# Kernel optimization log

Hardware: AMD Instinct MI355X
Metric: run time of the kernel (lower is better)

The kernel has to match this reference:

```python
import jax, jax.numpy as jnp
import numpy as np

B, NQ, NK, C = 8, 1024, 1024, 1024
H, DK, DV = 16, 64, 64


def setup_inputs() -> dict:
    key = jax.random.key(0)
    ks = jax.random.split(key, 10)
    queries = jax.random.normal(ks[0], (B, NQ, C), dtype=jnp.float32)
    keys_ = jax.random.normal(ks[1], (B, NK, C), dtype=jnp.float32)
    values = jax.random.normal(ks[2], (B, NK, C), dtype=jnp.float32)
    attention_mask = jax.random.randint(ks[3], (B, H, NQ, NK), 0, 2).astype(jnp.bool_)
    attention_weights = jax.random.uniform(ks[4], (B, H, NQ, NK), dtype=jnp.float32)
    std = 0.001  # init.normal_(m.weight, std=0.001), bias=0
    Wq = jax.random.normal(ks[5], (C, H * DK), dtype=jnp.float32) * std
    Wk = jax.random.normal(ks[6], (C, H * DK), dtype=jnp.float32) * std
    Wv = jax.random.normal(ks[7], (C, H * DV), dtype=jnp.float32) * std
    Wo = jax.random.normal(ks[8], (H * DV, C), dtype=jnp.float32) * std
    bq = jnp.zeros((H * DK,), jnp.float32)
    bk = jnp.zeros((H * DK,), jnp.float32)
    bv = jnp.zeros((H * DV,), jnp.float32)
    bo = jnp.zeros((C,), jnp.float32)
    return {"queries": queries, "keys": keys_, "values": values,
            "attention_mask": attention_mask, "attention_weights": attention_weights,
            "Wq": Wq, "bq": bq, "Wk": Wk, "bk": bk, "Wv": Wv, "bv": bv,
            "Wo": Wo, "bo": bo}


def reference(queries, keys, values, attention_mask, attention_weights,
              Wq, bq, Wk, bk, Wv, bv, Wo, bo):
    bs, nq, _ = queries.shape
    nk = keys.shape[1]
    # projections -> (b, h, n, d)
    q = (queries @ Wq + bq).reshape(bs, nq, H, DK).transpose(0, 2, 1, 3)
    k = (keys @ Wk + bk).reshape(bs, nk, H, DK).transpose(0, 2, 1, 3)
    v = (values @ Wv + bv).reshape(bs, nk, H, DV).transpose(0, 2, 1, 3)
    att = jnp.einsum('bhqd,bhkd->bhqk', q, k) / np.sqrt(DK).astype(np.float32)
    att = att * attention_weights
    att = jnp.where(attention_mask, -jnp.inf, att)
    att = jax.nn.softmax(att, axis=-1)
    # dropout is identity in eval mode
    out = jnp.einsum('bhqk,bhkd->bhqd', att, v)
    out = out.transpose(0, 2, 1, 3).reshape(bs, nq, H * DV)
    return out @ Wo + bo
```

## Files before the change

kernel.cpp:

```cpp
#include <hip/hip_runtime.h>
#include <hip/hip_bf16.h>

using short8 = __attribute__((ext_vector_type(8))) short;
using f32x4  = __attribute__((ext_vector_type(4))) float;

__device__ __forceinline__ unsigned short f2bf(float f) {
    union { float f; unsigned u; } x; x.f = f;
    unsigned r = x.u + 0x7FFFu + ((x.u >> 16) & 1u);
    return (unsigned short)(r >> 16);
}

__device__ __forceinline__ void gload_lds16(const void* g, void* l) {
    __builtin_amdgcn_global_load_lds(
        (const __attribute__((address_space(1))) unsigned int*)g,
        (__attribute__((address_space(3))) unsigned int*)l, 16, 0, 0);
}

__global__ void detect_mask_kernel(const unsigned int* __restrict__ m, int* __restrict__ flag) {
    if (threadIdx.x == 0) *flag = 0;
    __syncthreads();
    unsigned v = m[threadIdx.x];
    if (v > 1u) {
        atomicOr(flag, 1);
        if (v != 0x3F800000u) atomicOr(flag, 2);
    }
}

__global__ __launch_bounds__(256) void maskpack_kernel(
    const void* __restrict__ mask, const int* __restrict__ flag,
    unsigned long long* __restrict__ Mb, int nwords)
{
    const int l = threadIdx.x & 63;
    const int gwave = (int)((blockIdx.x * 256 + threadIdx.x) >> 6);
    const int nw = (int)((gridDim.x * 256) >> 6);
    const bool bytem = ((*flag) & 2) != 0;
    const unsigned char* m8 = (const unsigned char*)mask;
    const unsigned int* m32 = (const unsigned int*)mask;
    for (int w0 = gwave * 4; w0 < nwords; w0 += nw * 4) {
        unsigned v[4];
#pragma unroll
        for (int u = 0; u < 4; u++) {
            size_t e = (size_t)(w0 + u) * 64 + l;
            v[u] = bytem ? (unsigned)m8[e] : m32[e];
        }
#pragma unroll
        for (int u = 0; u < 4; u++) {
            unsigned long long b = __ballot(v[u] != 0u);
            if (l == 0) Mb[w0 + u] = b;
        }
    }
}

__global__ __launch_bounds__(256) void wconv_kernel(
    const float* __restrict__ W0, const float* __restrict__ W1,
    const float* __restrict__ W2, const float* __restrict__ W3,
    unsigned short* __restrict__ Wt)
{
    const int z = blockIdx.z;
    const float* W = (z == 0) ? W0 : ((z == 1) ? W1 : ((z == 2) ? W2 : W3));
    unsigned short* O = Wt + (size_t)z * 1024 * 1024;
    __shared__ float tile[64][68];
    const int t = threadIdx.x;
    const int k0 = blockIdx.x * 64, n0 = blockIdx.y * 64;
    const int rr = t >> 4, cc = t & 15;
#pragma unroll
    for (int i = 0; i < 4; i++) {
        int row = rr + i * 16;
        float4 v = *reinterpret_cast<const float4*>(W + (size_t)(k0 + row) * 1024 + n0 + cc * 4);
        *reinterpret_cast<float4*>(&tile[row][cc * 4]) = v;
    }
    __syncthreads();
#pragma unroll
    for (int i = 0; i < 4; i++) {
        int rn = rr + i * 16;
        ushort4 ov;
        ov.x = f2bf(tile[cc * 4 + 0][rn]);
        ov.y = f2bf(tile[cc * 4 + 1][rn]);
        ov.z = f2bf(tile[cc * 4 + 2][rn]);
        ov.w = f2bf(tile[cc * 4 + 3][rn]);
        *reinterpret_cast<ushort4*>(O + (size_t)(n0 + rn) * 1024 + k0 + cc * 4) = ov;
    }
}

__global__ __launch_bounds__(256) void aconv_kernel(
    const float* __restrict__ Aq, const float* __restrict__ Ak, const float* __restrict__ Av,
    unsigned short* __restrict__ Out)
{
    const int z = blockIdx.y;
    const float* A = (z == 0) ? Aq : ((z == 1) ? Ak : Av);
    unsigned short* O = Out + (size_t)z * 8192 * 1024;
    size_t i = ((size_t)blockIdx.x * 256 + threadIdx.x) * 8;
    float4 v0 = *reinterpret_cast<const float4*>(A + i);
    float4 v1 = *reinterpret_cast<const float4*>(A + i + 4);
    short8 o;
    o[0] = (short)f2bf(v0.x); o[1] = (short)f2bf(v0.y);
    o[2] = (short)f2bf(v0.z); o[3] = (short)f2bf(v0.w);
    o[4] = (short)f2bf(v1.x); o[5] = (short)f2bf(v1.y);
    o[6] = (short)f2bf(v1.z); o[7] = (short)f2bf(v1.w);
    *reinterpret_cast<short8*>(O + i) = o;
}

#define GEMM_IT(KT, RB, SB, DOST, WN)                                                       \
    {                                                                                       \
        if (DOST) {                                                                         \
            const int ko = ((KT) + 2) * 64;                                                 \
            gload_lds16(gA0 + ko, lA0_##SB); gload_lds16(gA1 + ko, lA1_##SB);               \
            gload_lds16(gB0 + ko, lB0_##SB); gload_lds16(gB1 + ko, lB1_##SB);               \
        }                                                                                   \
        short8 af[4], bfm[4];                                                               \
        _Pragma("unroll")                                                                   \
        for (int fr = 0; fr < 4; fr++)                                                      \
            af[fr] = *reinterpret_cast<const short8*>(rdA + (RB) * 8192 + fr * 1024);       \
        _Pragma("unroll")                                                                   \
        for (int fc = 0; fc < 4; fc++)                                                      \
            bfm[fc] = *reinterpret_cast<const short8*>(rdB + (RB) * 8192 + fc * 1024);      \
        _Pragma("unroll")                                                                   \
        for (int fr = 0; fr < 4; fr++)                                                      \
            _Pragma("unroll")                                                               \
            for (int fc = 0; fc < 4; fc++)                                                  \
                acc[fr][fc] = __builtin_amdgcn_mfma_f32_16x16x32_bf16(af[fr], bfm[fc], acc[fr][fc], 0, 0, 0); \
        asm volatile("s_waitcnt vmcnt(" #WN ")" ::: "memory");                              \
        __builtin_amdgcn_s_barrier();                                                       \
        __builtin_amdgcn_sched_barrier(0);                                                  \
    }

#define GEMM_IT_LAST(RB)                                                                    \
    {                                                                                       \
        short8 af[4], bfm[4];                                                               \
        _Pragma("unroll")                                                                   \
        for (int fr = 0; fr < 4; fr++)                                                      \
            af[fr] = *reinterpret_cast<const short8*>(rdA + (RB) * 8192 + fr * 1024);       \
        _Pragma("unroll")                                                                   \
        for (int fc = 0; fc < 4; fc++)                                                      \
            bfm[fc] = *reinterpret_cast<const short8*>(rdB + (RB) * 8192 + fc * 1024);      \
        _Pragma("unroll")                                                                   \
        for (int fr = 0; fr < 4; fr++)                                                      \
            _Pragma("unroll")                                                               \
            for (int fc = 0; fc < 4; fc++)                                                  \
                acc[fr][fc] = __builtin_amdgcn_mfma_f32_16x16x32_bf16(af[fr], bfm[fc], acc[fr][fc], 0, 0, 0); \
    }

#define GEMM_CORE(A_PTR, W_PTR)                                                             \
    __shared__ unsigned short Ab[3][4096];                                                  \
    __shared__ unsigned short Bb[3][4096];                                                  \
    const int tid = threadIdx.x, w = tid >> 6, l = tid & 63, l16 = l & 15, g = l >> 4;      \
    const int wr = w >> 1, wc = w & 1;                                                      \
    const int row0 = blockIdx.x * 128, col0 = blockIdx.y * 128;                             \
    const int offs = tid * 16;                                                              \
    const char* gA0 = (const char*)(A_PTR) + (size_t)(row0 + (offs >> 6)) * 2048 + (offs & 63);          \
    const char* gA1 = (const char*)(A_PTR) + (size_t)(row0 + ((offs + 4096) >> 6)) * 2048 + (offs & 63); \
    const char* gB0 = (const char*)(W_PTR) + (size_t)(col0 + (offs >> 6)) * 2048 + (offs & 63);          \
    const char* gB1 = (const char*)(W_PTR) + (size_t)(col0 + ((offs + 4096) >> 6)) * 2048 + (offs & 63); \
    char* lA0_0 = (char*)Ab[0] + w * 1024; char* lA1_0 = (char*)Ab[0] + 4096 + w * 1024;    \
    char* lA0_1 = (char*)Ab[1] + w * 1024; char* lA1_1 = (char*)Ab[1] + 4096 + w * 1024;    \
    char* lA0_2 = (char*)Ab[2] + w * 1024; char* lA1_2 = (char*)Ab[2] + 4096 + w * 1024;    \
    char* lB0_0 = (char*)Bb[0] + w * 1024; char* lB1_0 = (char*)Bb[0] + 4096 + w * 1024;    \
    char* lB0_1 = (char*)Bb[1] + w * 1024; char* lB1_1 = (char*)Bb[1] + 4096 + w * 1024;    \
    char* lB0_2 = (char*)Bb[2] + w * 1024; char* lB1_2 = (char*)Bb[2] + 4096 + w * 1024;    \
    const char* rdA = (char*)Ab[0] + (wr * 64 + l16) * 64 + g * 16;                         \
    const char* rdB = (char*)Bb[0] + (wc * 64 + l16) * 64 + g * 16;                         \
    f32x4 acc[4][4];                                                                        \
    _Pragma("unroll")                                                                       \
    for (int i = 0; i < 4; i++)                                                             \
        _Pragma("unroll")                                                                   \
        for (int j = 0; j < 4; j++) acc[i][j] = (f32x4){0.f, 0.f, 0.f, 0.f};                \
    gload_lds16(gA0, lA0_0); gload_lds16(gA1, lA1_0);                                       \
    gload_lds16(gB0, lB0_0); gload_lds16(gB1, lB1_0);                                       \
    gload_lds16(gA0 + 64, lA0_1); gload_lds16(gA1 + 64, lA1_1);                             \
    gload_lds16(gB0 + 64, lB0_1); gload_lds16(gB1 + 64, lB1_1);                             \
    asm volatile("s_waitcnt vmcnt(4)" ::: "memory");                                        \
    __builtin_amdgcn_s_barrier();                                                           \
    __builtin_amdgcn_sched_barrier(0);                                                      \
    for (int kt0 = 0; kt0 < 30; kt0 += 3) {                                                 \
        GEMM_IT(kt0 + 0, 0, 2, 1, 4)                                                        \
        GEMM_IT(kt0 + 1, 1, 0, 1, 4)                                                        \
        GEMM_IT(kt0 + 2, 2, 1, 1, 4)                                                        \
    }                                                                                       \
    GEMM_IT(30, 0, 0, 0, 0)                                                                 \
    GEMM_IT_LAST(1)

__global__ __launch_bounds__(256, 3) void gemm_proj_kernel(
    const unsigned short* __restrict__ Abf,
    const unsigned short* __restrict__ Wt,
    const float* __restrict__ bq, const float* __restrict__ bk, const float* __restrict__ bv,
    unsigned short* __restrict__ Out)
{
    const int z = blockIdx.z;
    const unsigned short* A = Abf + (size_t)z * 8192 * 1024;
    const unsigned short* Wz = Wt + (size_t)z * 1024 * 1024;
    const float* bias = (z == 0) ? bq : ((z == 1) ? bk : bv);
    unsigned short* Oz = Out + (size_t)z * 8 * 16 * 1024 * 64;

    GEMM_CORE(A, Wz)

#pragma unroll
    for (int fr = 0; fr < 4; fr++)
#pragma unroll
        for (int fc = 0; fc < 4; fc++)
#pragma unroll
            for (int r = 0; r < 4; r++) {
                int row = row0 + wr * 64 + fr * 16 + g * 4 + r;
                int col = col0 + wc * 64 + fc * 16 + l16;
                float val = acc[fr][fc][r] + bias[col];
                int bb = row >> 10, n = row & 1023;
                int h = col >> 6, d = col & 63;
                Oz[(((size_t)(bb * 16 + h)) * 1024 + n) * 64 + d] = f2bf(val);
            }
}

__global__ __launch_bounds__(256, 3) void gemm_out_kernel(
    const unsigned short* __restrict__ Ain,
    const unsigned short* __restrict__ Wto,
    const float* __restrict__ bo,
    float* __restrict__ Out)
{
    GEMM_CORE(Ain, Wto)

#pragma unroll
    for (int fr = 0; fr < 4; fr++)
#pragma unroll
        for (int fc = 0; fc < 4; fc++)
#pragma unroll
            for (int r = 0; r < 4; r++) {
                int row = row0 + wr * 64 + fr * 16 + g * 4 + r;
                int col = col0 + wc * 64 + fc * 16 + l16;
                Out[(size_t)row * 1024 + col] = acc[fr][fc][r] + bo[col];
            }
}

__global__ __launch_bounds__(256) void proj_f32_kernel(
    const float* __restrict__ Aq, const float* __restrict__ Ak, const float* __restrict__ Av,
    const unsigned short* __restrict__ Wt,
    const float* __restrict__ bq, const float* __restrict__ bk, const float* __restrict__ bv,
    unsigned short* __restrict__ Out)
{
    const int z = blockIdx.z;
    const float* A = (z == 0) ? Aq : ((z == 1) ? Ak : Av);
    const float* bias = (z == 0) ? bq : ((z == 1) ? bk : bv);
    const unsigned short* Wz = Wt + (size_t)z * 1024 * 1024;
    unsigned short* Oz = Out + (size_t)z * 8 * 16 * 1024 * 64;

    const int tid = threadIdx.x;
    const int w = tid >> 6, l = tid & 63;
    const int l16 = l & 15, g = l >> 4;
    const int rbase = blockIdx.x * 128 + w * 32;
    const int cbase = blockIdx.y * 64;

    f32x4 acc[2][4];
#pragma unroll
    for (int i = 0; i < 2; i++)
#pragma unroll
        for (int j = 0; j < 4; j++) acc[i][j] = (f32x4){0.f, 0.f, 0.f, 0.f};

#pragma unroll 2
    for (int k0 = 0; k0 < 1024; k0 += 32) {
        short8 a[2];
#pragma unroll
        for (int rf = 0; rf < 2; rf++) {
            const float* ap = A + (size_t)(rbase + rf * 16 + l16) * 1024 + k0 + g * 8;
            float4 v0 = *reinterpret_cast<const float4*>(ap);
            float4 v1 = *reinterpret_cast<const float4*>(ap + 4);
            short8 av;
            av[0] = (short)f2bf(v0.x); av[1] = (short)f2bf(v0.y);
            av[2] = (short)f2bf(v0.z); av[3] = (short)f2bf(v0.w);
            av[4] = (short)f2bf(v1.x); av[5] = (short)f2bf(v1.y);
            av[6] = (short)f2bf(v1.z); av[7] = (short)f2bf(v1.w);
            a[rf] = av;
        }
        short8 bfr[4];
#pragma unroll
        for (int cf = 0; cf < 4; cf++)
            bfr[cf] = *reinterpret_cast<const short8*>(Wz + (size_t)(cbase + cf * 16 + l16) * 1024 + k0 + g * 8);
#pragma unroll
        for (int rf = 0; rf < 2; rf++)
#pragma unroll
            for (int cf = 0; cf < 4; cf++)
                acc[rf][cf] = __builtin_amdgcn_mfma_f32_16x16x32_bf16(a[rf], bfr[cf], acc[rf][cf], 0, 0, 0);
    }

#pragma unroll
    for (int rf = 0; rf < 2; rf++)
#pragma unroll
        for (int cf = 0; cf < 4; cf++)
#pragma unroll
            for (int r = 0; r < 4; r++) {
                int row = rbase + rf * 16 + g * 4 + r;
                int col = cbase + cf * 16 + l16;
                float val = acc[rf][cf][r] + bias[col];
                int bb = row >> 10, n = row & 1023;
                int h = col >> 6, d = col & 63;
                Oz[(((size_t)(bb * 16 + h)) * 1024 + n) * 64 + d] = f2bf(val);
            }
}

__global__ __launch_bounds__(256) void vtrans_kernel(
    const unsigned short* __restrict__ Vs, unsigned short* __restrict__ Vt)
{
    const int bh = blockIdx.y;
    const int k0 = blockIdx.x * 64;
    const unsigned short* In = Vs + (size_t)bh * 1024 * 64;
    unsigned short* O = Vt + (size_t)bh * 64 * 1024;
    __shared__ unsigned short tile[64][72];
    const int t = threadIdx.x;
    {
        const int row = t >> 3;
        const int c8 = (t & 7) * 8;
#pragma unroll
        for (int i = 0; i < 2; i++) {
            int r = row + i * 32;
            short8 v = *reinterpret_cast<const short8*>(In + (size_t)(k0 + r) * 64 + c8);
            *reinterpret_cast<short8*>(&tile[r][c8]) = v;
        }
    }
    __syncthreads();
    {
        const int rd = t >> 4, c4 = (t & 15) * 4;
#pragma unroll
        for (int i = 0; i < 4; i++) {
            int d = rd + i * 16;
            ushort4 ov;
            ov.x = tile[c4 + 0][d];
            ov.y = tile[c4 + 1][d];
            ov.z = tile[c4 + 2][d];
            ov.w = tile[c4 + 3][d];
            *reinterpret_cast<ushort4*>(O + (size_t)d * 1024 + k0 + c4) = ov;
        }
    }
}

__global__ __launch_bounds__(512, 4) void attn_kernel(
    const unsigned short* __restrict__ Qs,
    const unsigned short* __restrict__ Ks,
    const unsigned short* __restrict__ Vt,
    const float* __restrict__ attw,
    const unsigned long long* __restrict__ Mb,
    unsigned short* __restrict__ AO)
{
    extern __shared__ char smem[];

    const int bid = blockIdx.x;
    const int xj = bid & 7, xp = bid >> 3;
    const int qt = xp & 7;
    const int gbh = (xp >> 3) * 8 + xj;
    const int h = gbh & 15, b = gbh >> 4;
    const int bh = b * 16 + h;

    const int tid = threadIdx.x, w = tid >> 6, l = tid & 63, l16 = l & 15, g = l >> 4;
    const int myq = qt * 128 + w * 16 + l16;

    const unsigned short* Qbh = Qs + (size_t)bh * 65536;
    const char* Kb = (const char*)(Ks + (size_t)bh * 65536);
    const char* Vb = (const char*)(Vt + (size_t)bh * 65536);
    const float* wrow = attw + ((size_t)bh * 1024 + myq) * 1024;
    const unsigned long long* mrow = Mb + ((size_t)bh * 1024 + myq) * 16;

    const int srow = w * 8 + (l >> 3);
    const int sinn = ((l & 7) * 16) ^ (((l >> 3) & 7) << 4);
    const char* gK = Kb + (size_t)srow * 128 + sinn;
    const char* gV = Vb + (size_t)srow * 2048 + sinn;

    const int rswz = (l16 & 7) << 4;
    const int krdA = l16 * 128 + ((g * 16) ^ rswz);
    const int krdB = l16 * 128 + ((64 + g * 16) ^ rswz);
    char* pw = smem + 49152 + w * 2304 + l16 * 144 + g * 8;
    char* pr = smem + 49152 + w * 2304 + l16 * 144 + g * 16;

    short8 qf0 = *reinterpret_cast<const short8*>(Qbh + (size_t)myq * 64 + g * 8);
    short8 qf1 = *reinterpret_cast<const short8*>(Qbh + (size_t)myq * 64 + 32 + g * 8);

    gload_lds16(gK, smem + 0 + w * 1024);
    gload_lds16(gV, smem + 24576 + w * 1024);

    float4 wv0[4], wv1[4], wv2[4];
    unsigned long long mb0, mb1, mb2;
#pragma unroll
    for (int cf = 0; cf < 4; cf++)
        wv0[cf] = *reinterpret_cast<const float4*>(wrow + cf * 16 + g * 4);
    mb0 = mrow[0];
#pragma unroll
    for (int cf = 0; cf < 4; cf++)
        wv1[cf] = *reinterpret_cast<const float4*>(wrow + 64 + cf * 16 + g * 4);
    mb1 = mrow[1];
    gload_lds16(gK + 8192, smem + 8192 + w * 1024);
    gload_lds16(gV + 128, smem + 24576 + 8192 + w * 1024);
#pragma unroll
    for (int cf = 0; cf < 4; cf++)
        wv2[cf] = *reinterpret_cast<const float4*>(wrow + 128 + cf * 16 + g * 4);
    mb2 = mrow[2];

    asm volatile("s_waitcnt vmcnt(7)" ::: "memory");
    __builtin_amdgcn_s_barrier();
    __builtin_amdgcn_sched_barrier(0);

    f32x4 accO[4];
#pragma unroll
    for (int j = 0; j < 4; j++) accO[j] = (f32x4){0.f, 0.f, 0.f, 0.f};
    float den = 0.f;

#define AITER(KT, B0, SB, WVC, MBC, DOST, DOREF, WN)                                        \
    {                                                                                       \
        if (DOST) {                                                                         \
            gload_lds16(gK + (size_t)((KT) + 2) * 8192, smem + (SB) * 8192 + w * 1024);     \
            gload_lds16(gV + (size_t)((KT) + 2) * 128, smem + 24576 + (SB) * 8192 + w * 1024); \
        }                                                                                   \
        _Pragma("unroll")                                                                   \
        for (int cf = 0; cf < 4; cf++) {                                                    \
            short8 k0 = *reinterpret_cast<const short8*>(smem + (B0) * 8192 + krdA + cf * 2048); \
            short8 k1 = *reinterpret_cast<const short8*>(smem + (B0) * 8192 + krdB + cf * 2048); \
            f32x4 s = (f32x4){0.f, 0.f, 0.f, 0.f};                                          \
            s = __builtin_amdgcn_mfma_f32_16x16x32_bf16(k0, qf0, s, 0, 0, 0);               \
            s = __builtin_amdgcn_mfma_f32_16x16x32_bf16(k1, qf1, s, 0, 0, 0);               \
            unsigned mn = (unsigned)((MBC) >> (cf * 16 + g * 4)) & 0xFu;                    \
            float p0 = (mn & 1u) ? 0.f : __expf(s[0] * 0.125f * (WVC)[cf].x);               \
            float p1 = (mn & 2u) ? 0.f : __expf(s[1] * 0.125f * (WVC)[cf].y);               \
            float p2 = (mn & 4u) ? 0.f : __expf(s[2] * 0.125f * (WVC)[cf].z);               \
            float p3 = (mn & 8u) ? 0.f : __expf(s[3] * 0.125f * (WVC)[cf].w);               \
            den += p0 + p1 + p2 + p3;                                                       \
            ushort4 pwv;                                                                    \
            pwv.x = f2bf(p0); pwv.y = f2bf(p1); pwv.z = f2bf(p2); pwv.w = f2bf(p3);         \
            *reinterpret_cast<ushort4*>(pw + cf * 32) = pwv;                                \
        }                                                                                   \
        if (DOREF) {                                                                        \
            _Pragma("unroll")                                                               \
            for (int cf = 0; cf < 4; cf++)                                                  \
                (WVC)[cf] = *reinterpret_cast<const float4*>(wrow + ((KT) + 3) * 64 + cf * 16 + g * 4); \
            (MBC) = mrow[(KT) + 3];                                                         \
        }                                                                                   \
        {                                                                                   \
            short8 pf0 = *reinterpret_cast<const short8*>(pr);                              \
            short8 pf1 = *reinterpret_cast<const short8*>(pr + 64);                         \
            _Pragma("unroll")                                                               \
            for (int cf = 0; cf < 4; cf++) {                                                \
                short8 v0 = *reinterpret_cast<const short8*>(smem + 24576 + (B0) * 8192 + krdA + cf * 2048); \
                short8 v1 = *reinterpret_cast<const short8*>(smem + 24576 + (B0) * 8192 + krdB + cf * 2048); \
                accO[cf] = __builtin_amdgcn_mfma_f32_16x16x32_bf16(pf0, v0, accO[cf], 0, 0, 0); \
                accO[cf] = __builtin_amdgcn_mfma_f32_16x16x32_bf16(pf1, v1, accO[cf], 0, 0, 0); \
            }                                                                               \
        }                                                                                   \
        asm volatile("s_waitcnt vmcnt(" #WN ")" ::: "memory");                              \
        __builtin_amdgcn_s_barrier();                                                       \
        __builtin_amdgcn_sched_barrier(0);                                                  \
    }

    for (int kb = 0; kb < 12; kb += 3) {
        AITER(kb + 0, 0, 2, wv0, mb0, 1, 1, 12)
        AITER(kb + 1, 1, 0, wv1, mb1, 1, 1, 12)
        AITER(kb + 2, 2, 1, wv2, mb2, 1, 1, 12)
    }
    AITER(12, 0, 2, wv0, mb0, 1, 1, 12)
    AITER(13, 1, 0, wv1, mb1, 1, 0, 7)
    AITER(14, 2, 1, wv2, mb2, 0, 0, 0)
    AITER(15, 0, 0, wv0, mb0, 0, 0, 0)
#undef AITER

    den += __shfl_xor(den, 16);
    den += __shfl_xor(den, 32);

#pragma unroll
    for (int r = 0; r < 4; r++) {
        float dr = __shfl(den, g * 4 + r);
        float inv = 1.0f / dr;
#pragma unroll
        for (int cf = 0; cf < 4; cf++) {
            int qrow = qt * 128 + w * 16 + g * 4 + r;
            int col = h * 64 + cf * 16 + l16;
            AO[((size_t)b * 1024 + qrow) * 1024 + col] = f2bf(accO[cf][r] * inv);
        }
    }
}

extern "C" void kernel_launch(void* const* d_in, const int* in_sizes, int n_in,
                              void* d_out, int out_size, void* d_ws, size_t ws_size,
                              hipStream_t stream)
{
    const float* queries = (const float*)d_in[0];
    const float* keys    = (const float*)d_in[1];
    const float* values  = (const float*)d_in[2];
    const void*  mask    = d_in[3];
    const float* attw    = (const float*)d_in[4];
    const float* Wq = (const float*)d_in[5];
    const float* bq = (const float*)d_in[6];
    const float* Wk = (const float*)d_in[7];
    const float* bk = (const float*)d_in[8];
    const float* Wv = (const float*)d_in[9];
    const float* bv = (const float*)d_in[10];
    const float* Wo = (const float*)d_in[11];
    const float* bo = (const float*)d_in[12];

    char* ws = (char*)d_ws;
    int* flag = (int*)ws;
    unsigned short* base = (unsigned short*)(ws + 256);
    const size_t M8 = (size_t)8 * 1024 * 1024;
    unsigned short* Qs  = base;
    unsigned short* Ksb = base + M8;
    unsigned short* Vs  = base + 2 * M8;
    unsigned short* Vtb = base + 3 * M8;
    unsigned short* AO  = base + 4 * M8;
    unsigned short* Wt  = base + 5 * M8;
    unsigned short* Abf = base + 5 * M8 + 4 * 1024 * 1024;
    unsigned long long* Mb = (unsigned long long*)Vs;
    const size_t need_abf = 256 + (5 * M8 + 4 * 1024 * 1024 + 3 * M8) * sizeof(unsigned short);
    const bool useAbf = ws_size >= need_abf;

    detect_mask_kernel<<<1, 256, 0, stream>>>((const unsigned int*)mask, flag);
    wconv_kernel<<<dim3(16, 16, 4), 256, 0, stream>>>(Wq, Wk, Wv, Wo, Wt);
    if (useAbf) {
        aconv_kernel<<<dim3(4096, 3), 256, 0, stream>>>(queries, keys, values, Abf);
        gemm_proj_kernel<<<dim3(64, 8, 3), 256, 0, stream>>>(Abf, Wt, bq, bk, bv, Qs);
    } else {
        proj_f32_kernel<<<dim3(64, 16, 3), 256, 0, stream>>>(queries, keys, values, Wt, bq, bk, bv, Qs);
    }
    vtrans_kernel<<<dim3(16, 128), 256, 0, stream>>>(Vs, Vtb);
    maskpack_kernel<<<dim3(2048), 256, 0, stream>>>(mask, flag, Mb, 2 * 1024 * 1024);
    attn_kernel<<<dim3(1024), 512, 67584, stream>>>(Qs, Ksb, Vtb, attw, Mb, AO);
    gemm_out_kernel<<<dim3(64, 8), 256, 0, stream>>>(AO, Wt + (size_t)3 * 1024 * 1024, bo, (float*)d_out);
}
```

Baseline: 430.8 us.

## Restructure attention loop to 128-key double-buffered tiles with swizzled P buffer

The attention kernel now processes 128 keys per iteration with a two-stage double buffer instead of 64 keys with a three-stage ring. K, V and the P scratch use larger XOR-swizzled LDS tiles, and PV is done as four 32-wide k-steps. The goal is fewer barriers and waits per key and better MFMA density per iteration. In exchange, LDS use grows to 96KB and launch bounds drop to one block, which likely cuts occupancy to about one block per CU and leaves less latency hiding for the attention-weight stream.

```diff
diff --git a/kernel.cpp b/kernel.cpp
--- a/kernel.cpp
+++ b/kernel.cpp
@@ -328,7 +328,7 @@
     }
 }
 
-__global__ __launch_bounds__(512, 4) void attn_kernel(
+__global__ __launch_bounds__(512, 1) void attn_kernel(
     const unsigned short* __restrict__ Qs,
     const unsigned short* __restrict__ Ks,
     const unsigned short* __restrict__ Vt,
@@ -354,41 +354,34 @@
     const float* wrow = attw + ((size_t)bh * 1024 + myq) * 1024;
     const unsigned long long* mrow = Mb + ((size_t)bh * 1024 + myq) * 16;
 
-    const int srow = w * 8 + (l >> 3);
-    const int sinn = ((l & 7) * 16) ^ (((l >> 3) & 7) << 4);
-    const char* gK = Kb + (size_t)srow * 128 + sinn;
-    const char* gV = Vb + (size_t)srow * 2048 + sinn;
-
-    const int rswz = (l16 & 7) << 4;
-    const int krdA = l16 * 128 + ((g * 16) ^ rswz);
-    const int krdB = l16 * 128 + ((64 + g * 16) ^ rswz);
-    char* pw = smem + 49152 + w * 2304 + l16 * 144 + g * 8;
-    char* pr = smem + 49152 + w * 2304 + l16 * 144 + g * 16;
+    const int kb_swz = ((l & 7) * 16) ^ ((l >> 3) << 4);
+    const char* gKb = Kb + (size_t)(w * 16 + (l >> 3)) * 128 + kb_swz;
+    const int vrow0 = w * 8 + (l >> 4);
+    const char* gVb0 = Vb + (size_t)vrow0 * 2048 + (((l & 15) * 16) ^ ((vrow0 & 7) << 4));
+    const char* gVb1 = Vb + (size_t)(vrow0 + 4) * 2048 + (((l & 15) * 16) ^ (((vrow0 + 4) & 7) << 4));
+
+    const int swz = (l16 & 7) << 4;
+    const int krdA = l16 * 128 + ((g * 16) ^ swz);
+    const int krdB = l16 * 128 + ((64 + g * 16) ^ swz);
+    char* const pbase = smem + 65536 + w * 4096 + l16 * 256;
+
+    gload_lds16(gKb, smem + w * 2048);
+    gload_lds16(gKb + 1024, smem + w * 2048 + 1024);
+    gload_lds16(gVb0, smem + 32768 + w * 2048);
+    gload_lds16(gVb1, smem + 32768 + w * 2048 + 1024);
+    __builtin_amdgcn_sched_barrier(0);
 
     short8 qf0 = *reinterpret_cast<const short8*>(Qbh + (size_t)myq * 64 + g * 8);
     short8 qf1 = *reinterpret_cast<const short8*>(Qbh + (size_t)myq * 64 + 32 + g * 8);
-
-    gload_lds16(gK, smem + 0 + w * 1024);
-    gload_lds16(gV, smem + 24576 + w * 1024);
-
-    float4 wv0[4], wv1[4], wv2[4];
-    unsigned long long mb0, mb1, mb2;
-#pragma unroll
-    for (int cf = 0; cf < 4; cf++)
-        wv0[cf] = *reinterpret_cast<const float4*>(wrow + cf * 16 + g * 4);
+    float4 wv[8];
+    unsigned long long mb0, mb1;
+#pragma unroll
+    for (int cf = 0; cf < 8; cf++)
+        wv[cf] = *reinterpret_cast<const float4*>(wrow + cf * 16 + g * 4);
     mb0 = mrow[0];
-#pragma unroll
-    for (int cf = 0; cf < 4; cf++)
-        wv1[cf] = *reinterpret_cast<const float4*>(wrow + 64 + cf * 16 + g * 4);
     mb1 = mrow[1];
-    gload_lds16(gK + 8192, smem + 8192 + w * 1024);
-    gload_lds16(gV + 128, smem + 24576 + 8192 + w * 1024);
-#pragma unroll
-    for (int cf = 0; cf < 4; cf++)
-        wv2[cf] = *reinterpret_cast<const float4*>(wrow + 128 + cf * 16 + g * 4);
-    mb2 = mrow[2];
-
-    asm volatile("s_waitcnt vmcnt(7)" ::: "memory");
+
+    asm volatile("s_waitcnt vmcnt(12)" ::: "memory");
     __builtin_amdgcn_s_barrier();
     __builtin_amdgcn_sched_barrier(0);
 
@@ -397,61 +390,64 @@
     for (int j = 0; j < 4; j++) accO[j] = (f32x4){0.f, 0.f, 0.f, 0.f};
     float den = 0.f;
 
-#define AITER(KT, B0, SB, WVC, MBC, DOST, DOREF, WN)                                        \
-    {                                                                                       \
-        if (DOST) {                                                                         \
-            gload_lds16(gK + (size_t)((KT) + 2) * 8192, smem + (SB) * 8192 + w * 1024);     \
-            gload_lds16(gV + (size_t)((KT) + 2) * 128, smem + 24576 + (SB) * 8192 + w * 1024); \
+#define ATTN_BODY(CURK)                                                                     \
+    _Pragma("unroll")                                                                       \
+    for (int cf = 0; cf < 8; cf++) {                                                        \
+        short8 k0 = *reinterpret_cast<const short8*>(smem + (CURK) + krdA + cf * 2048);     \
+        short8 k1 = *reinterpret_cast<const short8*>(smem + (CURK) + krdB + cf * 2048);     \
+        f32x4 s = (f32x4){0.f, 0.f, 0.f, 0.f};                                              \
+        s = __builtin_amdgcn_mfma_f32_16x16x32_bf16(k0, qf0, s, 0, 0, 0);                   \
+        s = __builtin_amdgcn_mfma_f32_16x16x32_bf16(k1, qf1, s, 0, 0, 0);                   \
+        unsigned mn = (unsigned)((cf < 4 ? mb0 >> (cf * 16 + g * 4)                         \
+                                         : mb1 >> ((cf - 4) * 16 + g * 4))) & 0xFu;         \
+        float p0 = (mn & 1u) ? 0.f : __expf(s[0] * 0.125f * wv[cf].x);                      \
+        float p1 = (mn & 2u) ? 0.f : __expf(s[1] * 0.125f * wv[cf].y);                      \
+        float p2 = (mn & 4u) ? 0.f : __expf(s[2] * 0.125f * wv[cf].z);                      \
+        float p3 = (mn & 8u) ? 0.f : __expf(s[3] * 0.125f * wv[cf].w);                      \
+        den += p0 + p1 + p2 + p3;                                                           \
+        ushort4 pwv;                                                                        \
+        pwv.x = f2bf(p0); pwv.y = f2bf(p1); pwv.z = f2bf(p2); pwv.w = f2bf(p3);             \
+        *reinterpret_cast<ushort4*>(pbase + ((cf * 32 + g * 8) ^ swz)) = pwv;               \
+    }
+
+#define ATTN_PV(CURV)                                                                       \
+    _Pragma("unroll")                                                                       \
+    for (int ks = 0; ks < 4; ks++) {                                                        \
+        short8 pf = *reinterpret_cast<const short8*>(pbase + ((ks * 64 + g * 16) ^ swz));   \
+        _Pragma("unroll")                                                                   \
+        for (int cd = 0; cd < 4; cd++) {                                                    \
+            short8 vf = *reinterpret_cast<const short8*>(                                   \
+                smem + 32768 + (CURV) + (cd * 16 + l16) * 256 + ((ks * 64 + g * 16) ^ swz));\
+            accO[cd] = __builtin_amdgcn_mfma_f32_16x16x32_bf16(pf, vf, accO[cd], 0, 0, 0);  \
         }                                                                                   \
-        _Pragma("unroll")                                                                   \
-        for (int cf = 0; cf < 4; cf++) {                                                    \
-            short8 k0 = *reinterpret_cast<const short8*>(smem + (B0) * 8192 + krdA + cf * 2048); \
-            short8 k1 = *reinterpret_cast<const short8*>(smem + (B0) * 8192 + krdB + cf * 2048); \
-            f32x4 s = (f32x4){0.f, 0.f, 0.f, 0.f};                                          \
-            s = __builtin_amdgcn_mfma_f32_16x16x32_bf16(k0, qf0, s, 0, 0, 0);               \
-            s = __builtin_amdgcn_mfma_f32_16x16x32_bf16(k1, qf1, s, 0, 0, 0);               \
-            unsigned mn = (unsigned)((MBC) >> (cf * 16 + g * 4)) & 0xFu;                    \
-            float p0 = (mn & 1u) ? 0.f : __expf(s[0] * 0.125f * (WVC)[cf].x);               \
-            float p1 = (mn & 2u) ? 0.f : __expf(s[1] * 0.125f * (WVC)[cf].y);               \
-            float p2 = (mn & 4u) ? 0.f : __expf(s[2] * 0.125f * (WVC)[cf].z);               \
-            float p3 = (mn & 8u) ? 0.f : __expf(s[3] * 0.125f * (WVC)[cf].w);               \
-            den += p0 + p1 + p2 + p3;                                                       \
-            ushort4 pwv;                                                                    \
-            pwv.x = f2bf(p0); pwv.y = f2bf(p1); pwv.z = f2bf(p2); pwv.w = f2bf(p3);         \
-            *reinterpret_cast<ushort4*>(pw + cf * 32) = pwv;                                \
-        }                                                                                   \
-        if (DOREF) {                                                                        \
-            _Pragma("unroll")                                                               \
-            for (int cf = 0; cf < 4; cf++)                                                  \
-                (WVC)[cf] = *reinterpret_cast<const float4*>(wrow + ((KT) + 3) * 64 + cf * 16 + g * 4); \
-            (MBC) = mrow[(KT) + 3];                                                         \
-        }                                                                                   \
-        {                                                                                   \
-            short8 pf0 = *reinterpret_cast<const short8*>(pr);                              \
-            short8 pf1 = *reinterpret_cast<const short8*>(pr + 64);                         \
-            _Pragma("unroll")                                                               \
-            for (int cf = 0; cf < 4; cf++) {                                                \
-                short8 v0 = *reinterpret_cast<const short8*>(smem + 24576 + (B0) * 8192 + krdA + cf * 2048); \
-                short8 v1 = *reinterpret_cast<const short8*>(smem + 24576 + (B0) * 8192 + krdB + cf * 2048); \
-                accO[cf] = __builtin_amdgcn_mfma_f32_16x16x32_bf16(pf0, v0, accO[cf], 0, 0, 0); \
-                accO[cf] = __builtin_amdgcn_mfma_f32_16x16x32_bf16(pf1, v1, accO[cf], 0, 0, 0); \
-            }                                                                               \
-        }                                                                                   \
-        asm volatile("s_waitcnt vmcnt(" #WN ")" ::: "memory");                              \
-        __builtin_amdgcn_s_barrier();                                                       \
-        __builtin_amdgcn_sched_barrier(0);                                                  \
-    }
-
-    for (int kb = 0; kb < 12; kb += 3) {
-        AITER(kb + 0, 0, 2, wv0, mb0, 1, 1, 12)
-        AITER(kb + 1, 1, 0, wv1, mb1, 1, 1, 12)
-        AITER(kb + 2, 2, 1, wv2, mb2, 1, 1, 12)
-    }
-    AITER(12, 0, 2, wv0, mb0, 1, 1, 12)
-    AITER(13, 1, 0, wv1, mb1, 1, 0, 7)
-    AITER(14, 2, 1, wv2, mb2, 0, 0, 0)
-    AITER(15, 0, 0, wv0, mb0, 0, 0, 0)
-#undef AITER
+    }
+
+    for (int t = 0; t < 7; t++) {
+        const int cur = (t & 1) * 16384, nxt = 16384 - cur;
+        gload_lds16(gKb + (size_t)(t + 1) * 16384, smem + nxt + w * 2048);
+        gload_lds16(gKb + (size_t)(t + 1) * 16384 + 1024, smem + nxt + w * 2048 + 1024);
+        gload_lds16(gVb0 + (size_t)(t + 1) * 256, smem + 32768 + nxt + w * 2048);
+        gload_lds16(gVb1 + (size_t)(t + 1) * 256, smem + 32768 + nxt + w * 2048 + 1024);
+        __builtin_amdgcn_sched_barrier(0);
+
+        ATTN_BODY(cur)
+
+#pragma unroll
+        for (int cf = 0; cf < 8; cf++)
+            wv[cf] = *reinterpret_cast<const float4*>(wrow + (t + 1) * 128 + cf * 16 + g * 4);
+        mb0 = mrow[2 * (t + 1)];
+        mb1 = mrow[2 * (t + 1) + 1];
+
+        ATTN_PV(cur)
+
+        asm volatile("s_waitcnt vmcnt(10)" ::: "memory");
+        __builtin_amdgcn_s_barrier();
+        __builtin_amdgcn_sched_barrier(0);
+    }
+    ATTN_BODY(16384)
+    ATTN_PV(16384)
+#undef ATTN_BODY
+#undef ATTN_PV
 
     den += __shfl_xor(den, 16);
     den += __shfl_xor(den, 32);
@@ -461,10 +457,10 @@
         float dr = __shfl(den, g * 4 + r);
         float inv = 1.0f / dr;
 #pragma unroll
-        for (int cf = 0; cf < 4; cf++) {
+        for (int cd = 0; cd < 4; cd++) {
             int qrow = qt * 128 + w * 16 + g * 4 + r;
-            int col = h * 64 + cf * 16 + l16;
-            AO[((size_t)b * 1024 + qrow) * 1024 + col] = f2bf(accO[cf][r] * inv);
+            int col = h * 64 + cd * 16 + l16;
+            AO[((size_t)b * 1024 + qrow) * 1024 + col] = f2bf(accO[cd][r] * inv);
         }
     }
 }
@@ -512,6 +508,6 @@
     }
     vtrans_kernel<<<dim3(16, 128), 256, 0, stream>>>(Vs, Vtb);
     maskpack_kernel<<<dim3(2048), 256, 0, stream>>>(mask, flag, Mb, 2 * 1024 * 1024);
-    attn_kernel<<<dim3(1024), 512, 67584, stream>>>(Qs, Ksb, Vtb, attw, Mb, AO);
+    attn_kernel<<<dim3(1024), 512, 98304, stream>>>(Qs, Ksb, Vtb, attw, Mb, AO);
     gemm_out_kernel<<<dim3(64, 8), 256, 0, stream>>>(AO, Wt + (size_t)3 * 1024 * 1024, bo, (float*)d_out);
 }
```

Measured after the change: 413.8 us. 3.9% less time.
